# Optimization experiments

Measured on AMD Instinct MI355X. Metric: run time of the kernel, lower is better.

## Reference

```python
import jax, jax.numpy as jnp
import numpy as np

K = 64        # top-k from init_kwargs
TAU = 1.0     # temperature at step=0: tau_start*(1-0) + tau_end*0


def setup_inputs() -> dict:
    key = jax.random.key(0)
    k1, k2 = jax.random.split(key)
    B, N = 2048, 8192
    logits = jax.random.normal(k1, (B, N), dtype=jnp.float32)
    # gumbels = -log(Exp(1)) == standard Gumbel noise
    gumbel_noise = jax.random.gumbel(k2, (B, N), dtype=jnp.float32)
    return {"logits": logits, "gumbel_noise": gumbel_noise}


def reference(logits, gumbel_noise):
    # training path of GumbelTopK (step=0 -> tau=TAU, hard=True)
    g = (logits + gumbel_noise) / TAU                       # [B, N]
    order = jnp.argsort(-g, axis=-1)                        # descending sort order
    sorted_g = jnp.take_along_axis(g, order, axis=-1)
    cumsum = jnp.cumsum(jax.nn.softmax(sorted_g, axis=-1), axis=-1)
    mask = (cumsum <= K).astype(sorted_g.dtype)             # NB: faithful to source (<= k)
    sorted_y = mask * jax.nn.softmax(sorted_g / TAU, axis=-1)
    # scatter back to original positions == gather by inverse permutation
    inv = jnp.argsort(order, axis=-1)
    y = jnp.take_along_axis(sorted_y, inv, axis=-1)         # [B, N]
    # hard straight-through: one-hot-k of y
    k = min(K, y.shape[-1])
    _, idx = jax.lax.top_k(y, k)                            # [B, k]
    rows = jnp.arange(y.shape[0])[:, None]
    y_hard = jnp.zeros_like(y).at[rows, idx].set(1.0)
    return jax.lax.stop_gradient(y_hard - y) + y
```

## Files before the change

### kernel.cpp

```cpp
#include <hip/hip_runtime.h>

constexpr int N = 8192;
constexpr int K = 64;
constexpr int THREADS = 256;
constexpr int WAVES = THREADS / 64;
constexpr int VEC = N / THREADS / 4;
constexpr int CAP = 1024;

__device__ __forceinline__ unsigned orderable(float f) {
    unsigned x = __float_as_uint(f);
    return (x & 0x80000000u) ? ~x : (x | 0x80000000u);
}

__global__ __launch_bounds__(THREADS, 8)
void gumbel_topk_onehot(const float* __restrict__ logits,
                        const float* __restrict__ noise,
                        float* __restrict__ out)
{
    __shared__ unsigned hist[2048];
    __shared__ unsigned cand[CAP];
    __shared__ unsigned wavesum[WAVES];
    __shared__ unsigned ccount;
    __shared__ unsigned sel_bin, sel_kth, sel_cnt;

    const int tid  = threadIdx.x;
    const int lane = tid & 63;
    const int wave = tid >> 6;
    const long long row = blockIdx.x;

    const float4* lrow = (const float4*)(logits + row * (long long)N);
    const float4* nrow = (const float4*)(noise  + row * (long long)N);

    {
        uint4 z = make_uint4(0,0,0,0);
        for (int i = tid; i < 512; i += THREADS) ((uint4*)hist)[i] = z;
    }
    if (tid == 0) ccount = 0;
    __syncthreads();
#pragma unroll
    for (int i = 0; i < VEC; ++i) {
        int idx = tid + i * THREADS;
        float4 a = lrow[idx];
        float4 b = nrow[idx];
        atomicAdd(&hist[orderable(a.x + b.x) >> 21], 1u);
        atomicAdd(&hist[orderable(a.y + b.y) >> 21], 1u);
        atomicAdd(&hist[orderable(a.z + b.z) >> 21], 1u);
        atomicAdd(&hist[orderable(a.w + b.w) >> 21], 1u);
    }
    __syncthreads();

    unsigned kth = K;

#define SELECT_BIN(BPT)                                                      \
    {                                                                        \
        unsigned p = 0;                                                      \
        _Pragma("unroll")                                                    \
        for (int j = 0; j < (BPT); ++j) p += hist[tid * (BPT) + j];          \
        unsigned s = p;                                                      \
        _Pragma("unroll")                                                    \
        for (int off = 1; off < 64; off <<= 1) {                             \
            unsigned v = __shfl_down(s, off);                                \
            if (lane + off < 64) s += v;                                     \
        }                                                                    \
        if (lane == 0) wavesum[wave] = s;                                    \
        __syncthreads();                                                     \
        unsigned S = s;                                                      \
        _Pragma("unroll")                                                    \
        for (int w = 0; w < WAVES; ++w) if (w > wave) S += wavesum[w];       \
        unsigned Snext = S - p;                                              \
        if (S >= kth && Snext < kth) {                                       \
            unsigned cum = Snext;                                            \
            for (int j = (BPT) - 1; j >= 0; --j) {                           \
                unsigned c = hist[tid * (BPT) + j];                          \
                if (cum + c >= kth) {                                        \
                    sel_bin = (unsigned)(tid * (BPT) + j);                   \
                    sel_kth = kth - cum;                                     \
                    sel_cnt = c;                                             \
                    break;                                                   \
                }                                                            \
                cum += c;                                                    \
            }                                                                \
        }                                                                    \
        __syncthreads();                                                     \
    }

    SELECT_BIN(8)
    const unsigned b1   = sel_bin;
    const unsigned cnt1 = sel_cnt;
    kth = sel_kth;
    __syncthreads();

    const bool use_cand = (cnt1 <= (unsigned)CAP);
    if (use_cand) {
#pragma unroll
        for (int i = 0; i < VEC; ++i) {
            int idx = tid + i * THREADS;
            float4 a = lrow[idx];
            float4 b = nrow[idx];
            unsigned k0 = orderable(a.x + b.x);
            unsigned k1 = orderable(a.y + b.y);
            unsigned k2 = orderable(a.z + b.z);
            unsigned k3 = orderable(a.w + b.w);
            if ((k0 >> 21) == b1) { unsigned p = atomicAdd(&ccount, 1u); if (p < (unsigned)CAP) cand[p] = k0 & 0x1FFFFFu; }
            if ((k1 >> 21) == b1) { unsigned p = atomicAdd(&ccount, 1u); if (p < (unsigned)CAP) cand[p] = k1 & 0x1FFFFFu; }
            if ((k2 >> 21) == b1) { unsigned p = atomicAdd(&ccount, 1u); if (p < (unsigned)CAP) cand[p] = k2 & 0x1FFFFFu; }
            if ((k3 >> 21) == b1) { unsigned p = atomicAdd(&ccount, 1u); if (p < (unsigned)CAP) cand[p] = k3 & 0x1FFFFFu; }
        }
    }

    __syncthreads();
    {
        uint4 z = make_uint4(0,0,0,0);
        for (int i = tid; i < 512; i += THREADS) ((uint4*)hist)[i] = z;
    }
    __syncthreads();
    if (use_cand) {
        for (int i = tid; i < (int)cnt1; i += THREADS)
            atomicAdd(&hist[cand[i] >> 10], 1u);
    } else {
#pragma unroll
        for (int i = 0; i < VEC; ++i) {
            int idx = tid + i * THREADS;
            float4 a = lrow[idx];
            float4 b = nrow[idx];
            unsigned k0 = orderable(a.x + b.x), k1 = orderable(a.y + b.y);
            unsigned k2 = orderable(a.z + b.z), k3 = orderable(a.w + b.w);
            if ((k0 >> 21) == b1) atomicAdd(&hist[(k0 >> 10) & 0x7FFu], 1u);
            if ((k1 >> 21) == b1) atomicAdd(&hist[(k1 >> 10) & 0x7FFu], 1u);
            if ((k2 >> 21) == b1) atomicAdd(&hist[(k2 >> 10) & 0x7FFu], 1u);
            if ((k3 >> 21) == b1) atomicAdd(&hist[(k3 >> 10) & 0x7FFu], 1u);
        }
    }
    __syncthreads();

    SELECT_BIN(8)
    const unsigned b2 = sel_bin;
    kth = sel_kth;
    __syncthreads();

    {
        uint4 z = make_uint4(0,0,0,0);
        for (int i = tid; i < 256; i += THREADS) ((uint4*)hist)[i] = z;
    }
    __syncthreads();
    if (use_cand) {
        for (int i = tid; i < (int)cnt1; i += THREADS) {
            unsigned cv = cand[i];
            if ((cv >> 10) == b2) atomicAdd(&hist[cv & 0x3FFu], 1u);
        }
    } else {
        const unsigned pfx = (b1 << 11) | b2;
#pragma unroll
        for (int i = 0; i < VEC; ++i) {
            int idx = tid + i * THREADS;
            float4 a = lrow[idx];
            float4 b = nrow[idx];
            unsigned k0 = orderable(a.x + b.x), k1 = orderable(a.y + b.y);
            unsigned k2 = orderable(a.z + b.z), k3 = orderable(a.w + b.w);
            if ((k0 >> 10) == pfx) atomicAdd(&hist[k0 & 0x3FFu], 1u);
            if ((k1 >> 10) == pfx) atomicAdd(&hist[k1 & 0x3FFu], 1u);
            if ((k2 >> 10) == pfx) atomicAdd(&hist[k2 & 0x3FFu], 1u);
            if ((k3 >> 10) == pfx) atomicAdd(&hist[k3 & 0x3FFu], 1u);
        }
    }
    __syncthreads();

    SELECT_BIN(4)
    const unsigned b3      = sel_bin;
    const unsigned take_eq = sel_kth;
    const unsigned c_eq    = sel_cnt;

    const unsigned T = (b1 << 21) | (b2 << 10) | b3;
    const bool fast = (take_eq == c_eq);

    float4* orow = (float4*)(out + row * (long long)N);
#pragma unroll
    for (int i = 0; i < VEC; ++i) {
        int idx = tid + i * THREADS;
        float4 a = lrow[idx];
        float4 b = nrow[idx];
        unsigned k0 = orderable(a.x + b.x), k1 = orderable(a.y + b.y);
        unsigned k2 = orderable(a.z + b.z), k3 = orderable(a.w + b.w);
        float4 o;
        o.x = (k0 > T || (fast && k0 == T)) ? 1.0f : 0.0f;
        o.y = (k1 > T || (fast && k1 == T)) ? 1.0f : 0.0f;
        o.z = (k2 > T || (fast && k2 == T)) ? 1.0f : 0.0f;
        o.w = (k3 > T || (fast && k3 == T)) ? 1.0f : 0.0f;
        orow[idx] = o;
    }

    if (!fast) {
        __syncthreads();
        if (tid == 0) {
            const float* lf = logits + row * (long long)N;
            const float* nf = noise  + row * (long long)N;
            float* of = out + row * (long long)N;
            unsigned c = 0;
            for (int i = 0; i < N; ++i) {
                if (orderable(lf[i] + nf[i]) == T) {
                    of[i] = 1.0f;
                    if (++c == take_eq) break;
                }
            }
        }
    }
#undef SELECT_BIN
}

extern "C" void kernel_launch(void* const* d_in, const int* in_sizes, int n_in,
                              void* d_out, int out_size, void* d_ws, size_t ws_size,
                              hipStream_t stream) {
    const float* logits = (const float*)d_in[0];
    const float* noise  = (const float*)d_in[1];
    float* out = (float*)d_out;
    const int rows = in_sizes[0] / N;
    gumbel_topk_onehot<<<rows, THREADS, 0, stream>>>(logits, noise, out);
}
```

Baseline: 199.3 us.

## Prefilter candidates above a fixed threshold and rank them directly in one pass

The kernel now reads each row once. It zeroes the output and collects every element whose perturbed score exceeds a fixed cutoff of 4.0 into shared memory, together with its index. When between K and CAP candidates survive, each candidate gets an exact rank by O(n^2) pairwise comparison with a lower-index tie-break, and the top K indices are written as ones. This removes the multi-pass radix histogram in the common case. The old radix select is kept as a fallback for rows where the candidate count falls outside that range. The fixed cutoff is tuned to the expected value distribution, and the launch-bounds occupancy hint drops from 8 to 4.

```diff
diff --git a/kernel.cpp b/kernel.cpp
--- a/kernel.cpp
+++ b/kernel.cpp
@@ -12,16 +12,19 @@
     return (x & 0x80000000u) ? ~x : (x | 0x80000000u);
 }
 
-__global__ __launch_bounds__(THREADS, 8)
+__global__ __launch_bounds__(THREADS, 4)
 void gumbel_topk_onehot(const float* __restrict__ logits,
                         const float* __restrict__ noise,
                         float* __restrict__ out)
 {
-    __shared__ unsigned hist[2048];
-    __shared__ unsigned cand[CAP];
+    __shared__ unsigned smem[2 * CAP];
     __shared__ unsigned wavesum[WAVES];
-    __shared__ unsigned ccount;
+    __shared__ unsigned cnt;
     __shared__ unsigned sel_bin, sel_kth, sel_cnt;
+
+    unsigned* candk = smem;
+    unsigned* candi = smem + CAP;
+    unsigned* hist  = smem;
 
     const int tid  = threadIdx.x;
     const int lane = tid & 63;
@@ -30,24 +33,45 @@
 
     const float4* lrow = (const float4*)(logits + row * (long long)N);
     const float4* nrow = (const float4*)(noise  + row * (long long)N);
-
-    {
-        uint4 z = make_uint4(0,0,0,0);
-        for (int i = tid; i < 512; i += THREADS) ((uint4*)hist)[i] = z;
-    }
-    if (tid == 0) ccount = 0;
-    __syncthreads();
-#pragma unroll
-    for (int i = 0; i < VEC; ++i) {
-        int idx = tid + i * THREADS;
-        float4 a = lrow[idx];
-        float4 b = nrow[idx];
-        atomicAdd(&hist[orderable(a.x + b.x) >> 21], 1u);
-        atomicAdd(&hist[orderable(a.y + b.y) >> 21], 1u);
-        atomicAdd(&hist[orderable(a.z + b.z) >> 21], 1u);
-        atomicAdd(&hist[orderable(a.w + b.w) >> 21], 1u);
-    }
-    __syncthreads();
+    float4* orow = (float4*)(out + row * (long long)N);
+
+    const unsigned T0 = orderable(4.0f);
+
+    if (tid == 0) cnt = 0;
+    __syncthreads();
+
+#pragma unroll
+    for (int i = 0; i < VEC; ++i) {
+        int idx = tid + i * THREADS;
+        float4 a = lrow[idx];
+        float4 b = nrow[idx];
+        unsigned k0 = orderable(a.x + b.x);
+        unsigned k1 = orderable(a.y + b.y);
+        unsigned k2 = orderable(a.z + b.z);
+        unsigned k3 = orderable(a.w + b.w);
+        orow[idx] = make_float4(0.f, 0.f, 0.f, 0.f);
+        if (k0 > T0) { unsigned p = atomicAdd(&cnt, 1u); if (p < CAP) { candk[p] = k0; candi[p] = 4u*idx + 0u; } }
+        if (k1 > T0) { unsigned p = atomicAdd(&cnt, 1u); if (p < CAP) { candk[p] = k1; candi[p] = 4u*idx + 1u; } }
+        if (k2 > T0) { unsigned p = atomicAdd(&cnt, 1u); if (p < CAP) { candk[p] = k2; candi[p] = 4u*idx + 2u; } }
+        if (k3 > T0) { unsigned p = atomicAdd(&cnt, 1u); if (p < CAP) { candk[p] = k3; candi[p] = 4u*idx + 3u; } }
+    }
+    __syncthreads();
+
+    const unsigned n = cnt;
+    if (n >= (unsigned)K && n <= (unsigned)CAP) {
+        for (unsigned t = tid; t < n; t += THREADS) {
+            unsigned kt = candk[t], it = candi[t];
+            unsigned rank = 0;
+            for (unsigned j = 0; j < n; ++j) {
+                unsigned kj = candk[j];
+                unsigned ij = candi[j];
+                rank += (kj > kt || (kj == kt && ij < it)) ? 1u : 0u;
+            }
+            if (rank < (unsigned)K)
+                out[row * (long long)N + it] = 1.0f;
+        }
+        return;
+    }
 
     unsigned kth = K;
 
@@ -84,55 +108,45 @@
         __syncthreads();                                                     \
     }
 
-    SELECT_BIN(8)
-    const unsigned b1   = sel_bin;
-    const unsigned cnt1 = sel_cnt;
-    kth = sel_kth;
-    __syncthreads();
-
-    const bool use_cand = (cnt1 <= (unsigned)CAP);
-    if (use_cand) {
-#pragma unroll
-        for (int i = 0; i < VEC; ++i) {
-            int idx = tid + i * THREADS;
-            float4 a = lrow[idx];
-            float4 b = nrow[idx];
-            unsigned k0 = orderable(a.x + b.x);
-            unsigned k1 = orderable(a.y + b.y);
-            unsigned k2 = orderable(a.z + b.z);
-            unsigned k3 = orderable(a.w + b.w);
-            if ((k0 >> 21) == b1) { unsigned p = atomicAdd(&ccount, 1u); if (p < (unsigned)CAP) cand[p] = k0 & 0x1FFFFFu; }
-            if ((k1 >> 21) == b1) { unsigned p = atomicAdd(&ccount, 1u); if (p < (unsigned)CAP) cand[p] = k1 & 0x1FFFFFu; }
-            if ((k2 >> 21) == b1) { unsigned p = atomicAdd(&ccount, 1u); if (p < (unsigned)CAP) cand[p] = k2 & 0x1FFFFFu; }
-            if ((k3 >> 21) == b1) { unsigned p = atomicAdd(&ccount, 1u); if (p < (unsigned)CAP) cand[p] = k3 & 0x1FFFFFu; }
-        }
-    }
-
-    __syncthreads();
     {
         uint4 z = make_uint4(0,0,0,0);
         for (int i = tid; i < 512; i += THREADS) ((uint4*)hist)[i] = z;
     }
     __syncthreads();
-    if (use_cand) {
-        for (int i = tid; i < (int)cnt1; i += THREADS)
-            atomicAdd(&hist[cand[i] >> 10], 1u);
-    } else {
-#pragma unroll
-        for (int i = 0; i < VEC; ++i) {
-            int idx = tid + i * THREADS;
-            float4 a = lrow[idx];
-            float4 b = nrow[idx];
-            unsigned k0 = orderable(a.x + b.x), k1 = orderable(a.y + b.y);
-            unsigned k2 = orderable(a.z + b.z), k3 = orderable(a.w + b.w);
-            if ((k0 >> 21) == b1) atomicAdd(&hist[(k0 >> 10) & 0x7FFu], 1u);
-            if ((k1 >> 21) == b1) atomicAdd(&hist[(k1 >> 10) & 0x7FFu], 1u);
-            if ((k2 >> 21) == b1) atomicAdd(&hist[(k2 >> 10) & 0x7FFu], 1u);
-            if ((k3 >> 21) == b1) atomicAdd(&hist[(k3 >> 10) & 0x7FFu], 1u);
-        }
-    }
-    __syncthreads();
-
+#pragma unroll
+    for (int i = 0; i < VEC; ++i) {
+        int idx = tid + i * THREADS;
+        float4 a = lrow[idx];
+        float4 b = nrow[idx];
+        atomicAdd(&hist[orderable(a.x + b.x) >> 21], 1u);
+        atomicAdd(&hist[orderable(a.y + b.y) >> 21], 1u);
+        atomicAdd(&hist[orderable(a.z + b.z) >> 21], 1u);
+        atomicAdd(&hist[orderable(a.w + b.w) >> 21], 1u);
+    }
+    __syncthreads();
+    SELECT_BIN(8)
+    const unsigned b1 = sel_bin;
+    kth = sel_kth;
+    __syncthreads();
+
+    {
+        uint4 z = make_uint4(0,0,0,0);
+        for (int i = tid; i < 512; i += THREADS) ((uint4*)hist)[i] = z;
+    }
+    __syncthreads();
+#pragma unroll
+    for (int i = 0; i < VEC; ++i) {
+        int idx = tid + i * THREADS;
+        float4 a = lrow[idx];
+        float4 b = nrow[idx];
+        unsigned k0 = orderable(a.x + b.x), k1 = orderable(a.y + b.y);
+        unsigned k2 = orderable(a.z + b.z), k3 = orderable(a.w + b.w);
+        if ((k0 >> 21) == b1) atomicAdd(&hist[(k0 >> 10) & 0x7FFu], 1u);
+        if ((k1 >> 21) == b1) atomicAdd(&hist[(k1 >> 10) & 0x7FFu], 1u);
+        if ((k2 >> 21) == b1) atomicAdd(&hist[(k2 >> 10) & 0x7FFu], 1u);
+        if ((k3 >> 21) == b1) atomicAdd(&hist[(k3 >> 10) & 0x7FFu], 1u);
+    }
+    __syncthreads();
     SELECT_BIN(8)
     const unsigned b2 = sel_bin;
     kth = sel_kth;
@@ -143,12 +157,7 @@
         for (int i = tid; i < 256; i += THREADS) ((uint4*)hist)[i] = z;
     }
     __syncthreads();
-    if (use_cand) {
-        for (int i = tid; i < (int)cnt1; i += THREADS) {
-            unsigned cv = cand[i];
-            if ((cv >> 10) == b2) atomicAdd(&hist[cv & 0x3FFu], 1u);
-        }
-    } else {
+    {
         const unsigned pfx = (b1 << 11) | b2;
 #pragma unroll
         for (int i = 0; i < VEC; ++i) {
@@ -164,7 +173,6 @@
         }
     }
     __syncthreads();
-
     SELECT_BIN(4)
     const unsigned b3      = sel_bin;
     const unsigned take_eq = sel_kth;
@@ -173,7 +181,6 @@
     const unsigned T = (b1 << 21) | (b2 << 10) | b3;
     const bool fast = (take_eq == c_eq);
 
-    float4* orow = (float4*)(out + row * (long long)N);
 #pragma unroll
     for (int i = 0; i < VEC; ++i) {
         int idx = tid + i * THREADS;
```

Result: slower. 250.7 us (+25.8%).
